# Kernel optimization log

Hardware: AMD Instinct MI355X
Metric: run time of the kernel (lower is better)

The kernel has to match this reference:

```python
import jax, jax.numpy as jnp
import numpy as np

REG = 0.1          # entropic regularisation (init kwarg)
N_ITERS = 200      # fixed Sinkhorn iteration count (POT numItermax-style)


def _cdist(x, y):
    # Euclidean (p=2) pairwise distances, shape (N, M)
    sq = (jnp.sum(x * x, axis=1)[:, None]
          + jnp.sum(y * y, axis=1)[None, :]
          - 2.0 * (x @ y.T))
    return jnp.sqrt(jnp.maximum(sq, 1e-12))


def _sinkhorn2_log(C, loga, logb, reg, n_iters):
    # Log-domain Sinkhorn: same fixed point as ot.sinkhorn2, numerically stable.
    f0 = jnp.zeros(C.shape[0], C.dtype)
    g0 = jnp.zeros(C.shape[1], C.dtype)

    def step(carry, _):
        f, g = carry
        f = reg * loga - reg * jax.scipy.special.logsumexp((g[None, :] - C) / reg, axis=1)
        g = reg * logb - reg * jax.scipy.special.logsumexp((f[:, None] - C) / reg, axis=0)
        return (f, g), None

    (f, g), _ = jax.lax.scan(step, (f0, g0), None, length=n_iters)
    P = jnp.exp((f[:, None] + g[None, :] - C) / reg)  # transport plan (N, M)
    return jnp.sum(P * C)                              # <P, C> = OT loss


def setup_inputs() -> dict:
    key = jax.random.key(0)
    k1, k2, k3, k4 = jax.random.split(key, 4)
    N, M, d = 4096, 8192, 512
    return {
        "descriptors": jax.random.normal(k1, (N, d), dtype=jnp.float32),
        "word_embeddings": jax.random.normal(k2, (M, d), dtype=jnp.float32),
        "aligned": jax.random.randint(k3, (N,), 0, M, dtype=jnp.int64),
        "tgt_probs": jax.random.uniform(k4, (M,), dtype=jnp.float32),
    }


def reference(descriptors, word_embeddings, aligned, tgt_probs):
    n = descriptors.shape[0]
    loga = jnp.full((n,), -jnp.log(jnp.asarray(n, descriptors.dtype)))  # uniform source
    b = tgt_probs / jnp.sum(tgt_probs)                                   # balanced: renormalise
    logb = jnp.log(b)

    C = _cdist(descriptors, word_embeddings)
    ot_loss = _sinkhorn2_log(C, loga, logb, REG, N_ITERS)

    # Supervised alignment MSE over aligned rows (aligned == -1 masked out)
    mask = (aligned != -1)
    idx = jnp.maximum(aligned, 0)
    diff = descriptors - word_embeddings[idx]            # (N, d)
    sq = jnp.sum(diff * diff, axis=1) * mask.astype(diff.dtype)
    cnt = jnp.sum(mask.astype(diff.dtype))
    d = descriptors.shape[1]
    distance_loss = jnp.where(cnt > 0, jnp.sum(sq) / (cnt * d), jnp.asarray(0.0, diff.dtype))

    return ot_loss + distance_loss
```

## Files before the change

### kernel.cpp

```cpp
#include <hip/hip_runtime.h>
#include <cmath>

#define REGP 0.1f
#define NIT 200
#define K2 14.4269504089f
#define CREF 28.5f
#define CLO  23.5f
#define QSV  (17.0f/255.0f)
#define QIV  15.0f
#define S2V  (QSV*K2)

#define NBLK 256
#define NTHR 512
#define NGRP 8
#define GSZ  (NBLK/NGRP)

typedef float  vf4  __attribute__((ext_vector_type(4)));
typedef short  vbf8 __attribute__((ext_vector_type(8)));
typedef unsigned short vu8 __attribute__((ext_vector_type(8)));

#if defined(__has_builtin) && __has_builtin(__builtin_amdgcn_exp2f)
#define EXP2F(x) __builtin_amdgcn_exp2f(x)
#else
#define EXP2F(x) exp2f(x)
#endif

static __device__ __forceinline__ unsigned short f2bf(float x) {
    unsigned int u = __float_as_uint(x);
    return (unsigned short)((u + 0x7FFFu + ((u >> 16) & 1u)) >> 16);
}

static __device__ __forceinline__ float wave_red_sum(float v) {
    #pragma unroll
    for (int o = 32; o > 0; o >>= 1) v += __shfl_xor(v, o, 64);
    return v;
}

static __device__ __forceinline__ void acc16(uint4 c, const vf4* gv, vf4& sacc) {
    #pragma unroll
    for (int d = 0; d < 4; ++d) {
        unsigned x = d == 0 ? c.x : d == 1 ? c.y : d == 2 ? c.z : c.w;
        vf4 g = gv[d];
        sacc[0] += EXP2F(fmaf((float)(x & 0xffu),         -S2V, g[0]));
        sacc[1] += EXP2F(fmaf((float)((x >> 8) & 0xffu),  -S2V, g[1]));
        sacc[2] += EXP2F(fmaf((float)((x >> 16) & 0xffu), -S2V, g[2]));
        sacc[3] += EXP2F(fmaf((float)(x >> 24),           -S2V, g[3]));
    }
}


static __device__ __forceinline__ void gbar(unsigned* bar, unsigned bi, int blk) {
    __syncthreads();
    if (threadIdx.x == 0) {
        int g = blk & (NGRP - 1);
        unsigned* cnt = bar + 32 * (1 + g);
        unsigned* gen = bar + 32 * (9 + g);
        unsigned old = __hip_atomic_fetch_add(cnt, 1u, __ATOMIC_RELAXED, __HIP_MEMORY_SCOPE_AGENT);
        if (old == bi * GSZ - 1u) {
            unsigned r = __hip_atomic_fetch_add(bar, 1u, __ATOMIC_RELAXED, __HIP_MEMORY_SCOPE_AGENT);
            if (r == bi * NGRP - 1u) {
                #pragma unroll
                for (int k = 0; k < NGRP; ++k)
                    __hip_atomic_store(bar + 32 * (9 + k), bi, __ATOMIC_RELAXED, __HIP_MEMORY_SCOPE_AGENT);
            } else {
                while (__hip_atomic_load(gen, __ATOMIC_RELAXED, __HIP_MEMORY_SCOPE_AGENT) < bi)
                    __builtin_amdgcn_s_sleep(4);
            }
        } else {
            while (__hip_atomic_load(gen, __ATOMIC_RELAXED, __HIP_MEMORY_SCOPE_AGENT) < bi)
                __builtin_amdgcn_s_sleep(4);
        }
    }
    __syncthreads();
}


template<int NG>
static __device__ __forceinline__ void stage_vk(const float* src, float* lds) {
    int t = threadIdx.x;
    int xr = (t >> 3) & 7;
    const unsigned long long* p = (const unsigned long long*)src;
    #pragma unroll
    for (int i = 0; i < NG; ++i) {
        int gr = i * NTHR + t;
        unsigned long long lo = __hip_atomic_load((unsigned long long*)&p[gr * 2],
                                                  __ATOMIC_RELAXED, __HIP_MEMORY_SCOPE_AGENT);
        unsigned long long hi = __hip_atomic_load((unsigned long long*)&p[gr * 2 + 1],
                                                  __ATOMIC_RELAXED, __HIP_MEMORY_SCOPE_AGENT);
        int pg = gr ^ xr;
        *(unsigned long long*)(lds + pg * 4)     = lo;
        *(unsigned long long*)(lds + pg * 4 + 2) = hi;
    }
}


__global__ void k_init(float* gk, float* scalars, unsigned* bar, int M) {
    int i = blockIdx.x * blockDim.x + threadIdx.x;
    if (i < M) gk[i] = 5.0f * K2;
    if (i < 8) scalars[i] = 0.f;
    if (i < 1024) bar[i] = 0u;
}

__global__ void k_convnorm(const float* __restrict__ X, unsigned short* __restrict__ Xb,
                           float* __restrict__ xx, int D) {
    int row = blockIdx.x, lane = threadIdx.x;
    const float* p = X + (size_t)row * D;
    unsigned short* q = Xb + (size_t)row * D;
    float sq = 0.f;
    for (int base = lane * 8; base < D; base += 512) {
        vf4 a = *(const vf4*)(p + base);
        vf4 b = *(const vf4*)(p + base + 4);
        vu8 o;
        #pragma unroll
        for (int e = 0; e < 4; ++e) {
            o[e]     = f2bf(a[e]);
            o[4 + e] = f2bf(b[e]);
            sq += a[e] * a[e] + b[e] * b[e];
        }
        *(vu8*)(q + base) = o;
    }
    sq = wave_red_sum(sq);
    if (lane == 0) xx[row] = sq;
}

__global__ void k_sumtgt(const float* __restrict__ t, float* scalars, int M) {
    __shared__ float red[4];
    float s = 0.f;
    for (int i = threadIdx.x; i < M; i += 256) s += t[i];
    s = wave_red_sum(s);
    if ((threadIdx.x & 63) == 0) red[threadIdx.x >> 6] = s;
    __syncthreads();
    if (threadIdx.x == 0) scalars[3] = logf(red[0] + red[1] + red[2] + red[3]);
}

__global__ void k_rlb(const float* __restrict__ tgt, const float* __restrict__ scalars,
                      float* __restrict__ rlb, int M) {
    int j = blockIdx.x * 256 + threadIdx.x;
    if (j < M) rlb[j] = REGP * (logf(tgt[j]) - scalars[3]);
}


__global__ __launch_bounds__(256, 2)
void k_gemm(const unsigned short* __restrict__ A, const unsigned short* __restrict__ B,
            const float* __restrict__ an, const float* __restrict__ bn,
            unsigned char* __restrict__ OUT, int ldo, int D) {
    int m0 = blockIdx.y * 128, n0 = blockIdx.x * 128;
    int wave = threadIdx.x >> 6, lane = threadIdx.x & 63;
    int lr = lane & 15, lk = (lane >> 4) * 8;
    const unsigned short* ax = A + (size_t)(m0 + wave * 32 + lr) * D + lk;
    const unsigned short* bx = B + (size_t)(n0 + lr) * D + lk;
    vf4 acc[2][8];
    #pragma unroll
    for (int r = 0; r < 2; ++r)
        #pragma unroll
        for (int c = 0; c < 8; ++c) acc[r][c] = (vf4){0.f, 0.f, 0.f, 0.f};

    for (int k = 0; k < D; k += 32) {
        vbf8 a0 = *(const vbf8*)(ax + k);
        vbf8 a1 = *(const vbf8*)(ax + 16 * D + k);
        #pragma unroll
        for (int c = 0; c < 8; ++c) {
            vbf8 b = *(const vbf8*)(bx + (size_t)c * 16 * D + k);
            acc[0][c] = __builtin_amdgcn_mfma_f32_16x16x32_bf16(a0, b, acc[0][c], 0, 0, 0);
            acc[1][c] = __builtin_amdgcn_mfma_f32_16x16x32_bf16(a1, b, acc[1][c], 0, 0, 0);
        }
    }
    int rbase = m0 + wave * 32 + (lane >> 4) * 4;
    #pragma unroll
    for (int r = 0; r < 2; ++r) {
        #pragma unroll
        for (int q = 0; q < 4; ++q) {
            int i = rbase + r * 16 + q;
            float xi = an[i];
            #pragma unroll
            for (int c = 0; c < 8; ++c) {
                int j = n0 + c * 16 + lr;
                float sq = xi + bn[j] - 2.f * acc[r][c][q];
                float cv = sqrtf(fmaxf(sq, 1e-12f));
                float qv = fminf(fmaxf((cv - CLO) * QIV, 0.f), 255.f);
                OUT[(size_t)i * ldo + j] = (unsigned char)(qv + 0.5f);
            }
        }
    }
}


template<int CHUNKS, int ROWITERS>
static __device__ __forceinline__ void phase(
        const unsigned char* __restrict__ Cm, const float* vlds,
        float* __restrict__ vout, float* vkout,
        const float* __restrict__ rlb, float rla,
        float outbase, float outkoff, int width, int rowbase) {
    int w = threadIdx.x >> 6, l = threadIdx.x & 63;
    int xr = (l >> 1) & 7;
    #pragma unroll
    for (int ri = 0; ri < ROWITERS; ++ri) {
        int rA = rowbase + ri * 16 + w * 2;
        const unsigned char* cpA = Cm + (size_t)rA * width + l * 16;
        const unsigned char* cpB = cpA + width;
        vf4 sA = (vf4){0.f,0.f,0.f,0.f}, sB = (vf4){0.f,0.f,0.f,0.f};
        #pragma unroll 2
        for (int ch = 0; ch < CHUNKS; ++ch) {
            uint4 a = *(const uint4*)(cpA + ch * 1024);
            uint4 b = *(const uint4*)(cpB + ch * 1024);
            int G0 = ch * 256 + l * 4;
            vf4 gv[4];
            #pragma unroll
            for (int q = 0; q < 4; ++q)
                gv[q] = *(const vf4*)(vlds + (size_t)((G0 + q) ^ xr) * 4);
            acc16(a, gv, sA);
            acc16(b, gv, sB);
        }
        float s0 = wave_red_sum(sA[0] + sA[1] + sA[2] + sA[3]);
        float s1 = wave_red_sum(sB[0] + sB[1] + sB[2] + sB[3]);
        if (l == 0) {
            #pragma unroll
            for (int rr = 0; rr < 2; ++rr) {
                int row = rA + rr;
                float s = rr == 0 ? s0 : s1;
                float off = rlb ? rlb[row] : rla;
                float val = off + outbase - log2f(s) * (1.0f / K2);
                vout[row] = val;
                float kv = (val + outkoff) * K2;
                __hip_atomic_store(&vkout[row], kv, __ATOMIC_RELAXED, __HIP_MEMORY_SCOPE_AGENT);
            }
        }
    }
}


__global__ __launch_bounds__(512, 2)
void k_sink(const unsigned char* __restrict__ C, const unsigned char* __restrict__ CT,
            float* __restrict__ f, float* __restrict__ g,
            float* fk, float* gk,
            const float* __restrict__ rlb, float rla,
            unsigned* bar, int N, int M) {
    __shared__ float vlds[8192];
    int blk = blockIdx.x;
    unsigned bi = 0;
    for (int it = 0; it < NIT; ++it) {
        stage_vk<4>(gk, vlds);
        __syncthreads();
        phase<8, 1>(C, vlds, f, fk, nullptr, rla, CREF, -CLO, M, blk * 16);
        gbar(bar, ++bi, blk);
        stage_vk<2>(fk, vlds);
        __syncthreads();
        phase<4, 2>(CT, vlds, g, gk, rlb, 0.f, 0.f, CREF - CLO, N, blk * 32);
        gbar(bar, ++bi, blk);
    }
}


__global__ __launch_bounds__(256)
void k_ot(const unsigned char* __restrict__ C, const float* __restrict__ f,
          const float* __restrict__ gk, float* __restrict__ scalars, int M) {
    int row = blockIdx.x * 4 + (threadIdx.x >> 6);
    int lane = threadIdx.x & 63;
    const unsigned char* cp = C + (size_t)row * M;
    float fk2 = (f[row] - CREF) * K2;
    float acc = 0.f;
    for (int base = lane * 16; base < M; base += 1024) {
        uint4 cw = *(const uint4*)(cp + base);
        #pragma unroll
        for (int d = 0; d < 4; ++d) {
            unsigned x = d == 0 ? cw.x : d == 1 ? cw.y : d == 2 ? cw.z : cw.w;
            vf4 g = *(const vf4*)(gk + base + d * 4);
            #pragma unroll
            for (int e = 0; e < 4; ++e) {
                float uf = (float)((x >> (8 * e)) & 0xffu);
                float t = fmaf(uf, -S2V, fk2 + g[e]);
                float cval = fmaf(uf, QSV, CLO);
                acc = fmaf(EXP2F(t), cval, acc);
            }
        }
    }
    acc = wave_red_sum(acc);
    if (lane == 0) atomicAdd(&scalars[0], acc);
}

__global__ void k_dist(const float* __restrict__ X, const float* __restrict__ Y,
                       const int* __restrict__ aligned, float* __restrict__ scalars, int D) {
    int i = blockIdx.x, lane = threadIdx.x;
    int a = aligned[i];
    if (a == -1) return;
    const float* xp = X + (size_t)i * D;
    const float* yp = Y + (size_t)a * D;
    float sq = 0.f;
    for (int base = lane * 8; base < D; base += 512) {
        vf4 x0 = *(const vf4*)(xp + base), x1 = *(const vf4*)(xp + base + 4);
        vf4 y0 = *(const vf4*)(yp + base), y1 = *(const vf4*)(yp + base + 4);
        #pragma unroll
        for (int e = 0; e < 4; ++e) {
            float d0 = x0[e] - y0[e], d1 = x1[e] - y1[e];
            sq += d0 * d0 + d1 * d1;
        }
    }
    sq = wave_red_sum(sq);
    if (lane == 0) { atomicAdd(&scalars[1], sq); atomicAdd(&scalars[2], 1.0f); }
}

__global__ void k_final(float* out, const float* __restrict__ scalars, int D) {
    float cnt = scalars[2];
    float dist = cnt > 0.f ? scalars[1] / (cnt * (float)D) : 0.f;
    out[0] = scalars[0] + dist;
}


extern "C" void kernel_launch(void* const* d_in, const int* in_sizes, int n_in,
                              void* d_out, int out_size, void* d_ws, size_t ws_size,
                              hipStream_t stream) {
    const float* X = (const float*)d_in[0];
    const float* Y = (const float*)d_in[1];
    const int* aligned = (const int*)d_in[2];
    const float* tgt = (const float*)d_in[3];
    int N = in_sizes[2];
    int M = in_sizes[3];
    int D = in_sizes[0] / N;
    float* out = (float*)d_out;

    char* w = (char*)d_ws;
    size_t off = 0;
    auto alloc = [&](size_t bytes) -> void* {
        void* p = w + off;
        off += (bytes + 255) & ~(size_t)255;
        return p;
    };
    unsigned short* Xb = (unsigned short*)alloc((size_t)N * D * 2);
    unsigned short* Yb = (unsigned short*)alloc((size_t)M * D * 2);
    unsigned char* C  = (unsigned char*)alloc((size_t)N * M);
    unsigned char* CT = (unsigned char*)alloc((size_t)N * M);
    float* xx  = (float*)alloc((size_t)N * 4);
    float* yy  = (float*)alloc((size_t)M * 4);
    float* f   = (float*)alloc((size_t)N * 4);
    float* g   = (float*)alloc((size_t)M * 4);
    float* fk  = (float*)alloc((size_t)N * 4);
    float* gk  = (float*)alloc((size_t)M * 4);
    float* rlb = (float*)alloc((size_t)M * 4);
    float* scalars = (float*)alloc(64);
    unsigned* bar = (unsigned*)alloc(4096);
    if (off > ws_size) return;

    float rla = -REGP * logf((float)N);

    k_init<<<dim3((M + 255) / 256), 256, 0, stream>>>(gk, scalars, bar, M);
    k_convnorm<<<dim3(N), 64, 0, stream>>>(X, Xb, xx, D);
    k_convnorm<<<dim3(M), 64, 0, stream>>>(Y, Yb, yy, D);
    k_sumtgt<<<1, 256, 0, stream>>>(tgt, scalars, M);
    k_rlb<<<dim3((M + 255) / 256), 256, 0, stream>>>(tgt, scalars, rlb, M);
    k_gemm<<<dim3(M / 128, N / 128), 256, 0, stream>>>(Xb, Yb, xx, yy, C,  M, D);
    k_gemm<<<dim3(N / 128, M / 128), 256, 0, stream>>>(Yb, Xb, yy, xx, CT, N, D);

    k_sink<<<dim3(NBLK), NTHR, 0, stream>>>(C, CT, f, g, fk, gk, rlb, rla, bar, N, M);

    k_ot<<<dim3(N / 4), 256, 0, stream>>>(C, f, gk, scalars, M);
    k_dist<<<dim3(N), 64, 0, stream>>>(X, Y, aligned, scalars, D);
    k_final<<<1, 1, 0, stream>>>(out, scalars, D);
}
```

Baseline: 4.333 ms.

## Keep C tile resident in LDS and compute column sums via partial reduction

Each persistent block now loads its 16-row slab of the quantized cost matrix into LDS once (128KB) and reuses it for both row and column Sinkhorn updates. The transposed matrix CT and its second GEMM are dropped. Column logsumexp is computed as per-block partial sums written to a global colpart buffer, then reduced across blocks after a grid barrier. This removes repeated global/L2 reads of C and CT every iteration, but adds a 256xM float partial buffer round-trip per iteration and limits occupancy to one block per CU.

Result: slower. 5.444 ms (+25.6%).

```diff
diff --git a/kernel.cpp b/kernel.cpp
--- a/kernel.cpp
+++ b/kernel.cpp
@@ -14,6 +14,13 @@
 #define NTHR 512
 #define NGRP 8
 #define GSZ  (NBLK/NGRP)
+
+#define SM_C    0
+#define SM_GKH  131072
+#define SM_FKL  147456
+#define SM_SRED 147520
+#define SM_RED2 147584
+#define SM_SIZE 149632
 
 typedef float  vf4  __attribute__((ext_vector_type(4)));
 typedef short  vbf8 __attribute__((ext_vector_type(8)));
@@ -75,25 +82,6 @@
 }
 
 
-template<int NG>
-static __device__ __forceinline__ void stage_vk(const float* src, float* lds) {
-    int t = threadIdx.x;
-    int xr = (t >> 3) & 7;
-    const unsigned long long* p = (const unsigned long long*)src;
-    #pragma unroll
-    for (int i = 0; i < NG; ++i) {
-        int gr = i * NTHR + t;
-        unsigned long long lo = __hip_atomic_load((unsigned long long*)&p[gr * 2],
-                                                  __ATOMIC_RELAXED, __HIP_MEMORY_SCOPE_AGENT);
-        unsigned long long hi = __hip_atomic_load((unsigned long long*)&p[gr * 2 + 1],
-                                                  __ATOMIC_RELAXED, __HIP_MEMORY_SCOPE_AGENT);
-        int pg = gr ^ xr;
-        *(unsigned long long*)(lds + pg * 4)     = lo;
-        *(unsigned long long*)(lds + pg * 4 + 2) = hi;
-    }
-}
-
-
 __global__ void k_init(float* gk, float* scalars, unsigned* bar, int M) {
     int i = blockIdx.x * blockDim.x + threadIdx.x;
     if (i < M) gk[i] = 5.0f * K2;
@@ -185,67 +173,122 @@
 }
 
 
-template<int CHUNKS, int ROWITERS>
-static __device__ __forceinline__ void phase(
-        const unsigned char* __restrict__ Cm, const float* vlds,
-        float* __restrict__ vout, float* vkout,
-        const float* __restrict__ rlb, float rla,
-        float outbase, float outkoff, int width, int rowbase) {
-    int w = threadIdx.x >> 6, l = threadIdx.x & 63;
+__global__ __launch_bounds__(NTHR, 1)
+void k_sink(const unsigned char* __restrict__ C, float* __restrict__ f,
+            float* gk, float* colpart, const float* __restrict__ rlb,
+            float rla, unsigned* bar, int N, int M) {
+    extern __shared__ char smem[];
+    unsigned char* cl = (unsigned char*)(smem + SM_C);
+    float* gkh  = (float*)(smem + SM_GKH);
+    float* fkl  = (float*)(smem + SM_FKL);
+    float* sred = (float*)(smem + SM_SRED);
+    float* red2 = (float*)(smem + SM_RED2);
+    int blk = blockIdx.x, tid = threadIdx.x;
+    int w = tid >> 6, l = tid & 63;
     int xr = (l >> 1) & 7;
-    #pragma unroll
-    for (int ri = 0; ri < ROWITERS; ++ri) {
-        int rA = rowbase + ri * 16 + w * 2;
-        const unsigned char* cpA = Cm + (size_t)rA * width + l * 16;
-        const unsigned char* cpB = cpA + width;
+
+    {
+        const unsigned char* src = C + (size_t)blk * 16 * M;
+        #pragma unroll
+        for (int r = 0; r < 16; ++r)
+            *(uint4*)(cl + r * 8192 + tid * 16) =
+                *(const uint4*)(src + (size_t)r * M + tid * 16);
+    }
+
+    unsigned bi = 0;
+    for (int it = 0; it < NIT; ++it) {
         vf4 sA = (vf4){0.f,0.f,0.f,0.f}, sB = (vf4){0.f,0.f,0.f,0.f};
-        #pragma unroll 2
-        for (int ch = 0; ch < CHUNKS; ++ch) {
-            uint4 a = *(const uint4*)(cpA + ch * 1024);
-            uint4 b = *(const uint4*)(cpB + ch * 1024);
-            int G0 = ch * 256 + l * 4;
-            vf4 gv[4];
-            #pragma unroll
-            for (int q = 0; q < 4; ++q)
-                gv[q] = *(const vf4*)(vlds + (size_t)((G0 + q) ^ xr) * 4);
-            acc16(a, gv, sA);
-            acc16(b, gv, sB);
+        const unsigned char* r0p = cl + (w * 2) * 8192;
+        const unsigned char* r1p = r0p + 8192;
+        #pragma unroll
+        for (int H = 0; H < 2; ++H) {
+            __syncthreads();
+            {
+                const unsigned long long* p = (const unsigned long long*)(gk + H * 4096);
+                #pragma unroll
+                for (int i = 0; i < 2; ++i) {
+                    int gr = i * NTHR + tid;
+                    unsigned long long lo = __hip_atomic_load(&p[(size_t)gr * 2],
+                                                __ATOMIC_RELAXED, __HIP_MEMORY_SCOPE_AGENT);
+                    unsigned long long hi = __hip_atomic_load(&p[(size_t)gr * 2 + 1],
+                                                __ATOMIC_RELAXED, __HIP_MEMORY_SCOPE_AGENT);
+                    int pg = gr ^ ((gr >> 3) & 7);
+                    *(unsigned long long*)(gkh + pg * 4)     = lo;
+                    *(unsigned long long*)(gkh + pg * 4 + 2) = hi;
+                }
+            }
+            __syncthreads();
+            #pragma unroll
+            for (int ch = 0; ch < 4; ++ch) {
+                uint4 a = *(const uint4*)(r0p + H * 4096 + ch * 1024 + l * 16);
+                uint4 b = *(const uint4*)(r1p + H * 4096 + ch * 1024 + l * 16);
+                int G0 = ch * 256 + l * 4;
+                vf4 gv[4];
+                #pragma unroll
+                for (int q = 0; q < 4; ++q)
+                    gv[q] = *(const vf4*)(gkh + (size_t)((G0 + q) ^ xr) * 4);
+                acc16(a, gv, sA);
+                acc16(b, gv, sB);
+            }
         }
         float s0 = wave_red_sum(sA[0] + sA[1] + sA[2] + sA[3]);
         float s1 = wave_red_sum(sB[0] + sB[1] + sB[2] + sB[3]);
-        if (l == 0) {
-            #pragma unroll
-            for (int rr = 0; rr < 2; ++rr) {
-                int row = rA + rr;
-                float s = rr == 0 ? s0 : s1;
-                float off = rlb ? rlb[row] : rla;
-                float val = off + outbase - log2f(s) * (1.0f / K2);
-                vout[row] = val;
-                float kv = (val + outkoff) * K2;
-                __hip_atomic_store(&vkout[row], kv, __ATOMIC_RELAXED, __HIP_MEMORY_SCOPE_AGENT);
-            }
-        }
-    }
-}
-
-
-__global__ __launch_bounds__(512, 2)
-void k_sink(const unsigned char* __restrict__ C, const unsigned char* __restrict__ CT,
-            float* __restrict__ f, float* __restrict__ g,
-            float* fk, float* gk,
-            const float* __restrict__ rlb, float rla,
-            unsigned* bar, int N, int M) {
-    __shared__ float vlds[8192];
-    int blk = blockIdx.x;
-    unsigned bi = 0;
-    for (int it = 0; it < NIT; ++it) {
-        stage_vk<4>(gk, vlds);
+        if (l == 0) { sred[w * 2] = s0; sred[w * 2 + 1] = s1; }
         __syncthreads();
-        phase<8, 1>(C, vlds, f, fk, nullptr, rla, CREF, -CLO, M, blk * 16);
+        if (tid < 16) {
+            float val = rla + CREF - log2f(sred[tid]) * (1.0f / K2);
+            f[blk * 16 + tid] = val;
+            fkl[tid] = (val - CLO) * K2;
+        }
+        __syncthreads();
+        {
+            float acc[16];
+            #pragma unroll
+            for (int k = 0; k < 16; ++k) acc[k] = 0.f;
+            const unsigned char* cp = cl + w * 1024 + l * 16;
+            #pragma unroll
+            for (int r = 0; r < 16; ++r) {
+                uint4 cw = *(const uint4*)(cp + r * 8192);
+                float fr = fkl[r];
+                #pragma unroll
+                for (int d = 0; d < 4; ++d) {
+                    unsigned x = d == 0 ? cw.x : d == 1 ? cw.y : d == 2 ? cw.z : cw.w;
+                    #pragma unroll
+                    for (int e = 0; e < 4; ++e)
+                        acc[d * 4 + e] += EXP2F(fmaf((float)((x >> (8 * e)) & 0xffu), -S2V, fr));
+                }
+            }
+            float* dst = colpart + (size_t)blk * M + w * 1024 + l * 16;
+            #pragma unroll
+            for (int k = 0; k < 16; k += 2) {
+                unsigned long long v = (unsigned long long)__float_as_uint(acc[k])
+                                     | ((unsigned long long)__float_as_uint(acc[k + 1]) << 32);
+                __hip_atomic_store((unsigned long long*)(dst + k), v,
+                                   __ATOMIC_RELAXED, __HIP_MEMORY_SCOPE_AGENT);
+            }
+        }
         gbar(bar, ++bi, blk);
-        stage_vk<2>(fk, vlds);
+        {
+            int c32 = tid & 31, p0 = tid >> 5;
+            int col = blk * 32 + c32;
+            float s = 0.f;
+            #pragma unroll
+            for (int k = 0; k < 16; ++k) {
+                int p = p0 + k * 16;
+                s += __hip_atomic_load(colpart + (size_t)p * M + col,
+                                       __ATOMIC_RELAXED, __HIP_MEMORY_SCOPE_AGENT);
+            }
+            red2[p0 * 32 + c32] = s;
+        }
         __syncthreads();
-        phase<4, 2>(CT, vlds, g, gk, rlb, 0.f, 0.f, CREF - CLO, N, blk * 32);
+        if (tid < 32) {
+            float s = 0.f;
+            #pragma unroll
+            for (int p = 0; p < 16; ++p) s += red2[p * 32 + tid];
+            int col = blk * 32 + tid;
+            float kv = (rlb[col] - log2f(s) * (1.0f / K2) + (CREF - CLO)) * K2;
+            __hip_atomic_store(gk + col, kv, __ATOMIC_RELAXED, __HIP_MEMORY_SCOPE_AGENT);
+        }
         gbar(bar, ++bi, blk);
     }
 }
@@ -328,12 +371,10 @@
     unsigned short* Xb = (unsigned short*)alloc((size_t)N * D * 2);
     unsigned short* Yb = (unsigned short*)alloc((size_t)M * D * 2);
     unsigned char* C  = (unsigned char*)alloc((size_t)N * M);
-    unsigned char* CT = (unsigned char*)alloc((size_t)N * M);
+    float* colpart = (float*)alloc((size_t)NBLK * M * 4);
     float* xx  = (float*)alloc((size_t)N * 4);
     float* yy  = (float*)alloc((size_t)M * 4);
     float* f   = (float*)alloc((size_t)N * 4);
-    float* g   = (float*)alloc((size_t)M * 4);
-    float* fk  = (float*)alloc((size_t)N * 4);
     float* gk  = (float*)alloc((size_t)M * 4);
     float* rlb = (float*)alloc((size_t)M * 4);
     float* scalars = (float*)alloc(64);
@@ -342,15 +383,17 @@
 
     float rla = -REGP * logf((float)N);
 
+    hipFuncSetAttribute((const void*)k_sink,
+                        hipFuncAttributeMaxDynamicSharedMemorySize, SM_SIZE);
+
     k_init<<<dim3((M + 255) / 256), 256, 0, stream>>>(gk, scalars, bar, M);
     k_convnorm<<<dim3(N), 64, 0, stream>>>(X, Xb, xx, D);
     k_convnorm<<<dim3(M), 64, 0, stream>>>(Y, Yb, yy, D);
     k_sumtgt<<<1, 256, 0, stream>>>(tgt, scalars, M);
     k_rlb<<<dim3((M + 255) / 256), 256, 0, stream>>>(tgt, scalars, rlb, M);
-    k_gemm<<<dim3(M / 128, N / 128), 256, 0, stream>>>(Xb, Yb, xx, yy, C,  M, D);
-    k_gemm<<<dim3(N / 128, M / 128), 256, 0, stream>>>(Yb, Xb, yy, xx, CT, N, D);
-
-    k_sink<<<dim3(NBLK), NTHR, 0, stream>>>(C, CT, f, g, fk, gk, rlb, rla, bar, N, M);
+    k_gemm<<<dim3(M / 128, N / 128), 256, 0, stream>>>(Xb, Yb, xx, yy, C, M, D);
+
+    k_sink<<<dim3(NBLK), NTHR, SM_SIZE, stream>>>(C, f, gk, colpart, rlb, rla, bar, N, M);
 
     k_ot<<<dim3(N / 4), 256, 0, stream>>>(C, f, gk, scalars, M);
     k_dist<<<dim3(N), 64, 0, stream>>>(X, Y, aligned, scalars, D);
```
